# Optimization experiments

Hardware: AMD Instinct MI355X
Metric: run time of the kernel (lower is better)

Reference implementation:

```python
import jax, jax.numpy as jnp
import numpy as np

N_NODES = 100000
N_EDGES = 625000
D = 128


def setup_inputs() -> dict:
    key = jax.random.key(0)
    ks = jax.random.split(key, 5)
    x = jax.random.normal(ks[0], (N_NODES, D), dtype=jnp.float32)
    edge_index = jax.random.randint(ks[1], (2, N_EDGES), 0, N_NODES, dtype=jnp.int64)
    scale = 1.0 / np.sqrt(D)
    W_neigh = jax.random.normal(ks[2], (D, D), dtype=jnp.float32) * scale
    W_self = jax.random.normal(ks[3], (D, D), dtype=jnp.float32) * scale
    b_self = jax.random.normal(ks[4], (D,), dtype=jnp.float32) * scale
    return {"x": x, "edge_index": edge_index, "W_neigh": W_neigh,
            "W_self": W_self, "b_self": b_self}


def reference(x, edge_index, W_neigh, W_self, b_self):
    src, dst = edge_index[0], edge_index[1]
    n = x.shape[0]
    # mean aggregation over incoming neighbors: segment-sum of x[src] into dst
    neigh = jax.ops.segment_sum(x[src], dst, num_segments=n)  # [N, D]
    counts = jax.ops.segment_sum(jnp.ones((src.shape[0],), dtype=x.dtype), dst,
                                 num_segments=n)  # [N]
    neigh = neigh / jnp.maximum(counts, 1.0)[:, None]
    # lin_self(x) + lin_neigh(neigh); nn.Linear computes x @ W.T + b
    return x @ W_self.T + b_self + neigh @ W_neigh.T
```

## Files before the change

kernel.cpp:

```cpp
#include <hip/hip_runtime.h>
#include <hip/hip_bf16.h>
#include <stdint.h>

#define DFEAT 128
#define CAP 40

typedef __attribute__((ext_vector_type(8))) short short8;
typedef __attribute__((ext_vector_type(4))) float f32x4;

static __device__ __forceinline__ unsigned short f2bf(float f) {
    union { float f; uint32_t u; } v; v.f = f;
    uint32_t u = v.u;
    u += 0x7FFFu + ((u >> 16) & 1u);
    return (unsigned short)(u >> 16);
}

static __device__ __forceinline__ float lo_bf(uint32_t u) {
    union { uint32_t u; float f; } v; v.u = u << 16; return v.f;
}
static __device__ __forceinline__ float hi_bf(uint32_t u) {
    union { uint32_t u; float f; } v; v.u = u & 0xFFFF0000u; return v.f;
}

static __device__ __forceinline__ short8 pack8(const float4& a, const float4& b) {
    short8 r;
    r[0] = (short)f2bf(a.x); r[1] = (short)f2bf(a.y);
    r[2] = (short)f2bf(a.z); r[3] = (short)f2bf(a.w);
    r[4] = (short)f2bf(b.x); r[5] = (short)f2bf(b.y);
    r[6] = (short)f2bf(b.z); r[7] = (short)f2bf(b.w);
    return r;
}

__global__ __launch_bounds__(256) void sage_prep(
    const float* __restrict__ x, unsigned short* __restrict__ xb, int total8,
    const int* __restrict__ ei, int* __restrict__ cur, int* __restrict__ nbr,
    int E) {
    int i = blockIdx.x * 256 + threadIdx.x;
    if (i < E) {
        int s = ei[i];
        int d = ei[E + i];
        int slot = atomicAdd(&cur[d], 1);
        if (slot < CAP) nbr[d * CAP + slot] = s;
    }
    if (i < total8) {
        float4 a = ((const float4*)x)[2 * i];
        float4 b = ((const float4*)x)[2 * i + 1];
        ((short8*)xb)[i] = pack8(a, b);
    }
}

__global__ __launch_bounds__(256) void sage_fused(
    const unsigned short* __restrict__ xb,
    const int* __restrict__ cur,
    const int* __restrict__ nbr,
    const float* __restrict__ Ws,
    const float* __restrict__ Wn,
    const float* __restrict__ bias,
    float* __restrict__ out,
    int N, int numTiles) {
    __shared__ unsigned short wlds[128 * 256];
    __shared__ unsigned short nlds[64 * 128];

    int t = threadIdx.x;
    #pragma unroll
    for (int it = 0; it < 16; ++it) {
        int id = it * 256 + t;
        int n  = id >> 5;
        int c  = id & 31;
        const float* srcw = (c < 16) ? (Ws + n * 128 + c * 8)
                                     : (Wn + n * 128 + (c - 16) * 8);
        int cs = c ^ (n & 7);
        float4 u0 = *(const float4*)(srcw);
        float4 u1 = *(const float4*)(srcw + 4);
        *(short8*)(wlds + n * 256 + cs * 8) = pack8(u0, u1);
    }
    __syncthreads();

    int lane = t & 63;
    int wave = t >> 6;
    int m = lane & 15;
    int q = lane >> 4;
    int grp = wave * 4 + q;
    int sl = lane & 15;

    for (int tile = blockIdx.x; tile < numTiles; tile += gridDim.x) {
        #pragma unroll
        for (int k = 0; k < 4; ++k) {
            int rl = grp + k * 16;
            int node = tile * 64 + rl;
            float acc[8] = {0.f, 0.f, 0.f, 0.f, 0.f, 0.f, 0.f, 0.f};
            int degTrue = 0;
            if (node < N) {
                degTrue = cur[node];
                int deg = degTrue < CAP ? degTrue : CAP;
                const int* nb = nbr + (size_t)node * CAP;
                for (int j0 = 0; j0 < deg; j0 += 8) {
                    int last = deg - 1;
                    int idx[8];
                    #pragma unroll
                    for (int kk = 0; kk < 8; ++kk) {
                        int jj = j0 + kk;
                        idx[kk] = nb[jj < deg ? jj : last];
                    }
                    uint4 u[8];
                    #pragma unroll
                    for (int kk = 0; kk < 8; ++kk)
                        u[kk] = ((const uint4*)(xb + (size_t)idx[kk] * DFEAT))[sl];
                    #pragma unroll
                    for (int kk = 0; kk < 8; ++kk) {
                        if (j0 + kk < deg) {
                            acc[0] += lo_bf(u[kk].x); acc[1] += hi_bf(u[kk].x);
                            acc[2] += lo_bf(u[kk].y); acc[3] += hi_bf(u[kk].y);
                            acc[4] += lo_bf(u[kk].z); acc[5] += hi_bf(u[kk].z);
                            acc[6] += lo_bf(u[kk].w); acc[7] += hi_bf(u[kk].w);
                        }
                    }
                }
            }
            float inv = 1.0f / fmaxf((float)degTrue, 1.0f);
            uint4 o;
            o.x = (uint32_t)f2bf(acc[0] * inv) | ((uint32_t)f2bf(acc[1] * inv) << 16);
            o.y = (uint32_t)f2bf(acc[2] * inv) | ((uint32_t)f2bf(acc[3] * inv) << 16);
            o.z = (uint32_t)f2bf(acc[4] * inv) | ((uint32_t)f2bf(acc[5] * inv) << 16);
            o.w = (uint32_t)f2bf(acc[6] * inv) | ((uint32_t)f2bf(acc[7] * inv) << 16);
            int us = sl ^ (rl & 7);
            *(uint4*)(nlds + rl * 128 + us * 8) = o;
        }
        __syncthreads();

        int arow = tile * 64 + wave * 16 + m;
        bool valid = arow < N;

        short8 afrag[8];
        if (valid) {
            const unsigned short* xr = xb + (size_t)arow * DFEAT;
            #pragma unroll
            for (int tt = 0; tt < 4; ++tt)
                afrag[tt] = *(const short8*)(xr + tt * 32 + q * 8);
        } else {
            #pragma unroll
            for (int tt = 0; tt < 4; ++tt) {
                short8 z = {0, 0, 0, 0, 0, 0, 0, 0};
                afrag[tt] = z;
            }
        }
        int rloc = wave * 16 + m;
        #pragma unroll
        for (int tt = 0; tt < 4; ++tt) {
            int u = tt * 4 + q;
            int us = u ^ (m & 7);
            afrag[4 + tt] = *(const short8*)(nlds + rloc * 128 + us * 8);
        }

        int orow_base = tile * 64 + wave * 16 + q * 4;
        #pragma unroll
        for (int jt = 0; jt < 8; ++jt) {
            f32x4 c4 = {0.f, 0.f, 0.f, 0.f};
            int n = jt * 16 + m;
            #pragma unroll
            for (int tt = 0; tt < 8; ++tt) {
                int c = tt * 4 + q;
                int cs = c ^ (n & 7);
                short8 bfrag = *(const short8*)(wlds + n * 256 + cs * 8);
                c4 = __builtin_amdgcn_mfma_f32_16x16x32_bf16(afrag[tt], bfrag, c4, 0, 0, 0);
            }
            float bv = bias[n];
            #pragma unroll
            for (int r = 0; r < 4; ++r) {
                int orow = orow_base + r;
                if (orow < N) out[(size_t)orow * DFEAT + n] = c4[r] + bv;
            }
        }
        __syncthreads();
    }
}

extern "C" void kernel_launch(void* const* d_in, const int* in_sizes, int n_in,
                              void* d_out, int out_size, void* d_ws, size_t ws_size,
                              hipStream_t stream) {
    const float* x  = (const float*)d_in[0];
    const int*   ei = (const int*)d_in[1];
    const float* Wn = (const float*)d_in[2];
    const float* Ws = (const float*)d_in[3];
    const float* b  = (const float*)d_in[4];
    float* out = (float*)d_out;

    int N = in_sizes[0] / DFEAT;
    int E = in_sizes[1] / 2;

    int* cur = (int*)d_ws;
    int* nbr = cur + N;
    unsigned short* xbuf = (unsigned short*)(nbr + (size_t)N * CAP);

    hipMemsetAsync(cur, 0, (size_t)N * sizeof(int), stream);

    int total8 = N * DFEAT / 8;
    int prepThreads = total8 > E ? total8 : E;
    sage_prep<<<(prepThreads + 255) / 256, 256, 0, stream>>>(
        x, xbuf, total8, ei, cur, nbr, E);

    int numTiles = (N + 63) / 64;
    sage_fused<<<512, 256, 0, stream>>>(xbuf, cur, nbr, Ws, Wn, b, out, N, numTiles);
}
```

Measured before the change: 208.5 us.

## Drop LDS from fused kernel, pre-convert weights, split prep, gather in MFMA layout

Weight bf16 conversion moves into a separate convert kernel writing a global buffer, and edge bucketing becomes its own kernel handling two edges per thread. The fused kernel no longer uses shared memory or barriers. Each wave gathers neighbour rows directly into the MFMA A-fragment layout, so the aggregation result stays in registers and there is no LDS round trip. B fragments now come from global or L2 memory instead of LDS, and one block per 64-node tile replaces the persistent grid, aiming for higher occupancy and less synchronisation. The trade-offs are one extra launch, more register pressure from the 32 accumulators, and more global-memory weight reads.

```diff
diff --git a/kernel.cpp b/kernel.cpp
--- a/kernel.cpp
+++ b/kernel.cpp
@@ -31,147 +31,142 @@
     return r;
 }
 
-__global__ __launch_bounds__(256) void sage_prep(
+__global__ __launch_bounds__(256) void sage_fill(
+    const int* __restrict__ ei, int* __restrict__ cur, int* __restrict__ nbr,
+    int E, int EH) {
+    int et = blockIdx.x * 256 + threadIdx.x;
+    if (et >= EH) return;
+    int e0 = et;
+    int e1 = et + EH;
+    bool has1 = e1 < E;
+    int s0 = ei[e0];
+    int d0 = ei[E + e0];
+    int s1 = 0, d1 = 0;
+    if (has1) { s1 = ei[e1]; d1 = ei[E + e1]; }
+    int slot0 = atomicAdd(&cur[d0], 1);
+    int slot1 = has1 ? atomicAdd(&cur[d1], 1) : CAP;
+    if (slot0 < CAP) nbr[(size_t)d0 * CAP + slot0] = s0;
+    if (has1 && slot1 < CAP) nbr[(size_t)d1 * CAP + slot1] = s1;
+}
+
+__global__ __launch_bounds__(256) void sage_convert(
     const float* __restrict__ x, unsigned short* __restrict__ xb, int total8,
-    const int* __restrict__ ei, int* __restrict__ cur, int* __restrict__ nbr,
-    int E) {
+    const float* __restrict__ Ws, const float* __restrict__ Wn,
+    unsigned short* __restrict__ wb) {
     int i = blockIdx.x * 256 + threadIdx.x;
-    if (i < E) {
-        int s = ei[i];
-        int d = ei[E + i];
-        int slot = atomicAdd(&cur[d], 1);
-        if (slot < CAP) nbr[d * CAP + slot] = s;
-    }
     if (i < total8) {
         float4 a = ((const float4*)x)[2 * i];
         float4 b = ((const float4*)x)[2 * i + 1];
         ((short8*)xb)[i] = pack8(a, b);
-    }
-}
-
-__global__ __launch_bounds__(256) void sage_fused(
+    } else if (i < total8 + 4096) {
+        int j = i - total8;
+        int n = j >> 5;
+        int c = j & 31;
+        const float* srcw = (c < 16) ? (Ws + n * 128 + c * 8)
+                                     : (Wn + n * 128 + (c - 16) * 8);
+        float4 u0 = *(const float4*)(srcw);
+        float4 u1 = *(const float4*)(srcw + 4);
+        *(short8*)(wb + n * 256 + c * 8) = pack8(u0, u1);
+    }
+}
+
+__global__ __launch_bounds__(256, 4) void sage_fused(
     const unsigned short* __restrict__ xb,
     const int* __restrict__ cur,
     const int* __restrict__ nbr,
-    const float* __restrict__ Ws,
-    const float* __restrict__ Wn,
+    const unsigned short* __restrict__ wb,
     const float* __restrict__ bias,
-    float* __restrict__ out,
-    int N, int numTiles) {
-    __shared__ unsigned short wlds[128 * 256];
-    __shared__ unsigned short nlds[64 * 128];
-
-    int t = threadIdx.x;
-    #pragma unroll
-    for (int it = 0; it < 16; ++it) {
-        int id = it * 256 + t;
-        int n  = id >> 5;
-        int c  = id & 31;
-        const float* srcw = (c < 16) ? (Ws + n * 128 + c * 8)
-                                     : (Wn + n * 128 + (c - 16) * 8);
-        int cs = c ^ (n & 7);
-        float4 u0 = *(const float4*)(srcw);
-        float4 u1 = *(const float4*)(srcw + 4);
-        *(short8*)(wlds + n * 256 + cs * 8) = pack8(u0, u1);
-    }
-    __syncthreads();
-
-    int lane = t & 63;
-    int wave = t >> 6;
+    float* __restrict__ out, int N) {
+    int wave = threadIdx.x >> 6;
+    int lane = threadIdx.x & 63;
     int m = lane & 15;
     int q = lane >> 4;
-    int grp = wave * 4 + q;
-    int sl = lane & 15;
-
-    for (int tile = blockIdx.x; tile < numTiles; tile += gridDim.x) {
-        #pragma unroll
-        for (int k = 0; k < 4; ++k) {
-            int rl = grp + k * 16;
-            int node = tile * 64 + rl;
-            float acc[8] = {0.f, 0.f, 0.f, 0.f, 0.f, 0.f, 0.f, 0.f};
-            int degTrue = 0;
-            if (node < N) {
-                degTrue = cur[node];
-                int deg = degTrue < CAP ? degTrue : CAP;
-                const int* nb = nbr + (size_t)node * CAP;
-                for (int j0 = 0; j0 < deg; j0 += 8) {
-                    int last = deg - 1;
-                    int idx[8];
-                    #pragma unroll
-                    for (int kk = 0; kk < 8; ++kk) {
-                        int jj = j0 + kk;
-                        idx[kk] = nb[jj < deg ? jj : last];
-                    }
-                    uint4 u[8];
-                    #pragma unroll
-                    for (int kk = 0; kk < 8; ++kk)
-                        u[kk] = ((const uint4*)(xb + (size_t)idx[kk] * DFEAT))[sl];
-                    #pragma unroll
-                    for (int kk = 0; kk < 8; ++kk) {
-                        if (j0 + kk < deg) {
-                            acc[0] += lo_bf(u[kk].x); acc[1] += hi_bf(u[kk].x);
-                            acc[2] += lo_bf(u[kk].y); acc[3] += hi_bf(u[kk].y);
-                            acc[4] += lo_bf(u[kk].z); acc[5] += hi_bf(u[kk].z);
-                            acc[6] += lo_bf(u[kk].w); acc[7] += hi_bf(u[kk].w);
-                        }
-                    }
+    int rbase = (blockIdx.x * 4 + wave) * 16;
+    if (rbase >= N) return;
+    int node = rbase + m;
+    bool vn = node < N;
+
+    float acc[4][8];
+    #pragma unroll
+    for (int tt = 0; tt < 4; ++tt)
+        #pragma unroll
+        for (int j = 0; j < 8; ++j) acc[tt][j] = 0.f;
+
+    int degTrue = 0;
+    if (vn) {
+        degTrue = cur[node];
+        int deg = degTrue < CAP ? degTrue : CAP;
+        const int* nb = nbr + (size_t)node * CAP;
+        for (int j0 = 0; j0 < deg; j0 += 2) {
+            int last = deg - 1;
+            int j1 = (j0 + 1 < deg) ? j0 + 1 : last;
+            int i0 = nb[j0];
+            int i1 = nb[j1];
+            const uint4* r0 = (const uint4*)(xb + (size_t)i0 * DFEAT);
+            const uint4* r1 = (const uint4*)(xb + (size_t)i1 * DFEAT);
+            uint4 u0[4], u1[4];
+            #pragma unroll
+            for (int tt = 0; tt < 4; ++tt) u0[tt] = r0[tt * 4 + q];
+            #pragma unroll
+            for (int tt = 0; tt < 4; ++tt) u1[tt] = r1[tt * 4 + q];
+            #pragma unroll
+            for (int tt = 0; tt < 4; ++tt) {
+                acc[tt][0] += lo_bf(u0[tt].x); acc[tt][1] += hi_bf(u0[tt].x);
+                acc[tt][2] += lo_bf(u0[tt].y); acc[tt][3] += hi_bf(u0[tt].y);
+                acc[tt][4] += lo_bf(u0[tt].z); acc[tt][5] += hi_bf(u0[tt].z);
+                acc[tt][6] += lo_bf(u0[tt].w); acc[tt][7] += hi_bf(u0[tt].w);
+            }
+            if (j0 + 1 < deg) {
+                #pragma unroll
+                for (int tt = 0; tt < 4; ++tt) {
+                    acc[tt][0] += lo_bf(u1[tt].x); acc[tt][1] += hi_bf(u1[tt].x);
+                    acc[tt][2] += lo_bf(u1[tt].y); acc[tt][3] += hi_bf(u1[tt].y);
+                    acc[tt][4] += lo_bf(u1[tt].z); acc[tt][5] += hi_bf(u1[tt].z);
+                    acc[tt][6] += lo_bf(u1[tt].w); acc[tt][7] += hi_bf(u1[tt].w);
                 }
             }
-            float inv = 1.0f / fmaxf((float)degTrue, 1.0f);
-            uint4 o;
-            o.x = (uint32_t)f2bf(acc[0] * inv) | ((uint32_t)f2bf(acc[1] * inv) << 16);
-            o.y = (uint32_t)f2bf(acc[2] * inv) | ((uint32_t)f2bf(acc[3] * inv) << 16);
-            o.z = (uint32_t)f2bf(acc[4] * inv) | ((uint32_t)f2bf(acc[5] * inv) << 16);
-            o.w = (uint32_t)f2bf(acc[6] * inv) | ((uint32_t)f2bf(acc[7] * inv) << 16);
-            int us = sl ^ (rl & 7);
-            *(uint4*)(nlds + rl * 128 + us * 8) = o;
-        }
-        __syncthreads();
-
-        int arow = tile * 64 + wave * 16 + m;
-        bool valid = arow < N;
-
-        short8 afrag[8];
-        if (valid) {
-            const unsigned short* xr = xb + (size_t)arow * DFEAT;
-            #pragma unroll
-            for (int tt = 0; tt < 4; ++tt)
-                afrag[tt] = *(const short8*)(xr + tt * 32 + q * 8);
-        } else {
-            #pragma unroll
-            for (int tt = 0; tt < 4; ++tt) {
-                short8 z = {0, 0, 0, 0, 0, 0, 0, 0};
-                afrag[tt] = z;
-            }
-        }
-        int rloc = wave * 16 + m;
+        }
+    }
+
+    float inv = 1.0f / fmaxf((float)degTrue, 1.0f);
+    short8 afrag[8];
+    #pragma unroll
+    for (int tt = 0; tt < 4; ++tt) {
+        short8 r;
+        #pragma unroll
+        for (int j = 0; j < 8; ++j) r[j] = (short)f2bf(acc[tt][j] * inv);
+        afrag[4 + tt] = r;
+    }
+
+    if (vn) {
+        const unsigned short* xr = xb + (size_t)node * DFEAT;
+        #pragma unroll
+        for (int tt = 0; tt < 4; ++tt)
+            afrag[tt] = *(const short8*)(xr + tt * 32 + q * 8);
+    } else {
         #pragma unroll
         for (int tt = 0; tt < 4; ++tt) {
-            int u = tt * 4 + q;
-            int us = u ^ (m & 7);
-            afrag[4 + tt] = *(const short8*)(nlds + rloc * 128 + us * 8);
-        }
-
-        int orow_base = tile * 64 + wave * 16 + q * 4;
-        #pragma unroll
-        for (int jt = 0; jt < 8; ++jt) {
-            f32x4 c4 = {0.f, 0.f, 0.f, 0.f};
-            int n = jt * 16 + m;
-            #pragma unroll
-            for (int tt = 0; tt < 8; ++tt) {
-                int c = tt * 4 + q;
-                int cs = c ^ (n & 7);
-                short8 bfrag = *(const short8*)(wlds + n * 256 + cs * 8);
-                c4 = __builtin_amdgcn_mfma_f32_16x16x32_bf16(afrag[tt], bfrag, c4, 0, 0, 0);
-            }
-            float bv = bias[n];
-            #pragma unroll
-            for (int r = 0; r < 4; ++r) {
-                int orow = orow_base + r;
-                if (orow < N) out[(size_t)orow * DFEAT + n] = c4[r] + bv;
-            }
-        }
-        __syncthreads();
+            short8 z = {0, 0, 0, 0, 0, 0, 0, 0};
+            afrag[tt] = z;
+        }
+    }
+
+    #pragma unroll
+    for (int jt = 0; jt < 8; ++jt) {
+        f32x4 c4 = {0.f, 0.f, 0.f, 0.f};
+        int n = jt * 16 + m;
+        const unsigned short* wr = wb + (size_t)n * 256;
+        #pragma unroll
+        for (int tt = 0; tt < 8; ++tt) {
+            short8 bfrag = *(const short8*)(wr + tt * 32 + q * 8);
+            c4 = __builtin_amdgcn_mfma_f32_16x16x32_bf16(afrag[tt], bfrag, c4, 0, 0, 0);
+        }
+        float bv = bias[n];
+        #pragma unroll
+        for (int r = 0; r < 4; ++r) {
+            int orow = rbase + q * 4 + r;
+            if (orow < N) out[(size_t)orow * DFEAT + n] = c4[r] + bv;
+        }
     }
 }
 
@@ -191,14 +186,17 @@
     int* cur = (int*)d_ws;
     int* nbr = cur + N;
     unsigned short* xbuf = (unsigned short*)(nbr + (size_t)N * CAP);
+    unsigned short* wb = xbuf + (size_t)N * DFEAT;
 
     hipMemsetAsync(cur, 0, (size_t)N * sizeof(int), stream);
 
     int total8 = N * DFEAT / 8;
-    int prepThreads = total8 > E ? total8 : E;
-    sage_prep<<<(prepThreads + 255) / 256, 256, 0, stream>>>(
-        x, xbuf, total8, ei, cur, nbr, E);
-
-    int numTiles = (N + 63) / 64;
-    sage_fused<<<512, 256, 0, stream>>>(xbuf, cur, nbr, Ws, Wn, b, out, N, numTiles);
-}
+    sage_convert<<<(total8 + 4096 + 255) / 256, 256, 0, stream>>>(
+        x, xbuf, total8, Ws, Wn, wb);
+
+    int EH = (E + 1) / 2;
+    sage_fill<<<(EH + 255) / 256, 256, 0, stream>>>(ei, cur, nbr, E, EH);
+
+    int numBlocks = (N + 63) / 64;
+    sage_fused<<<numBlocks, 256, 0, stream>>>(xbuf, cur, nbr, wb, b, out, N);
+}
```

Result: slower. 226.4 us (+8.6%).
